# Kernel tuning notes

Hardware: AMD Instinct MI355X
Metric: run time of the kernel (lower is better)

## Reference

```python
import jax, jax.numpy as jnp
import numpy as np

HEADS = 8
DIM_HEAD = 40
SCALE = DIM_HEAD ** -0.5


def setup_inputs() -> dict:
    key = jax.random.key(0)
    ks = jax.random.split(key, 6)
    B, S, D = 2, 4096, 320  # batch, seq (64x64 latent), query_dim
    inner = HEADS * DIM_HEAD  # 320
    s = 0.02
    return {
        "x": jax.random.normal(ks[0], (B, S, D), jnp.float32),
        "Wq": jax.random.normal(ks[1], (inner, D), jnp.float32) * s,
        "Wk": jax.random.normal(ks[2], (inner, D), jnp.float32) * s,
        "Wv": jax.random.normal(ks[3], (inner, D), jnp.float32) * s,
        "Wout": jax.random.normal(ks[4], (D, inner), jnp.float32) * s,
        "bout": jnp.zeros((D,), jnp.float32),
    }


def _split_heads(t):
    # [B, S, h*d] -> [B, h, S, d]
    B, S, _ = t.shape
    return t.reshape(B, S, HEADS, DIM_HEAD).transpose(0, 2, 1, 3)


def reference(x, Wq, Wk, Wv, Wout, bout):
    # self-attention path (context=None): k/v come from x
    q = _split_heads(x @ Wq.T)  # [B,h,S,d]
    k = _split_heads(x @ Wk.T)
    v = _split_heads(x @ Wv.T)
    # scores: materialized O(S^2) attention as in the torch einsum
    attn = jax.nn.softmax(jnp.einsum('bhid,bhjd->bhij', q, k) * SCALE, axis=-1)
    out = jnp.einsum('bhij,bhjd->bhid', attn, v)  # [B,h,S,d]
    B, _, S, _ = out.shape
    out = out.transpose(0, 2, 1, 3).reshape(B, S, HEADS * DIM_HEAD)
    return out @ Wout.T + bout  # to_out (dropout=0 -> identity)
```

## Files before the change

### kernel.cpp

```cpp
#include <hip/hip_runtime.h>

#define HEADS 8
#define DHEAD 40
#define SEQ   4096
#define BATCH 2
#define INNER 320
#define NBH   16
#define QSCALE ((float)(0.15811388300841897 * 1.4426950408889634))

typedef _Float16 f16;
typedef __attribute__((ext_vector_type(2)))  __fp16   fp16x2;
typedef __attribute__((ext_vector_type(4)))  _Float16 half4;
typedef __attribute__((ext_vector_type(8)))  _Float16 half8;
typedef __attribute__((ext_vector_type(16))) float    f32x16;

#if __has_builtin(__builtin_amdgcn_exp2f)
#define EXP2F(x) __builtin_amdgcn_exp2f(x)
#else
#define EXP2F(x) exp2f(x)
#endif

union H8 { half8 h8; fp16x2 p2[4]; uint4 u4; };

#define XN4   (BATCH * SEQ * INNER / 4)
#define WQKV4 (3 * INNER * INNER / 4)
#define WOUT4 (INNER * INNER / 4)
#define CONV_TOTAL (XN4 + WQKV4 + WOUT4)

__global__ __launch_bounds__(256)
void convert_kernel(const float* __restrict__ x,
                    const float* __restrict__ Wq,
                    const float* __restrict__ Wk,
                    const float* __restrict__ Wv,
                    const float* __restrict__ Wout,
                    f16* __restrict__ xh, f16* __restrict__ wh,
                    f16* __restrict__ wouth)
{
    int i = blockIdx.x * 256 + threadIdx.x;
    if (i >= CONV_TOTAL) return;
    float4 v;
    f16* dst;
    float sc = 1.0f;
    if (i < XN4) {
        v = ((const float4*)x)[i];
        dst = xh + 4 * (size_t)i;
    } else if (i < XN4 + WQKV4) {
        int j = i - XN4;
        if (j < 25600)      { v = ((const float4*)Wq)[j]; sc = QSCALE; }
        else if (j < 51200) { v = ((const float4*)Wk)[j - 25600]; }
        else                { v = ((const float4*)Wv)[j - 51200]; }
        dst = wh + 4 * (size_t)j;
    } else {
        int j = i - XN4 - WQKV4;
        v = ((const float4*)Wout)[j];
        dst = wouth + 4 * (size_t)j;
    }
    H8 u;
    u.p2[0] = __builtin_amdgcn_cvt_pkrtz(v.x * sc, v.y * sc);
    u.p2[1] = __builtin_amdgcn_cvt_pkrtz(v.z * sc, v.w * sc);
    *(uint2*)dst = make_uint2(u.u4.x, u.u4.y);
}

#define QSTR 72

__global__ __launch_bounds__(256)
void qkv_gemm_kernel(const f16* __restrict__ xh, const f16* __restrict__ wh,
                     f16* __restrict__ q, f16* __restrict__ k,
                     f16* __restrict__ vt)
{
    __shared__ f16 lds[(64 + 192) * QSTR];
    f16* As = lds;
    f16* Bs = lds + 64 * QSTR;

    const int tid = threadIdx.x;
    const int nb0 = blockIdx.x * 64;
    const int m0  = blockIdx.y * 64;
    const int wave = tid >> 6, lane = tid & 63, m = lane & 31, half = lane >> 5;
    const int mw = wave >> 1, nw = wave & 1;

    f32x16 acc[3];
    #pragma unroll
    for (int i = 0; i < 16; i++) { acc[0][i] = 0.f; acc[1][i] = 0.f; acc[2][i] = 0.f; }

    for (int k0 = 0; k0 < 320; k0 += 64) {
        __syncthreads();
        #pragma unroll
        for (int u = 0; u < 2; u++) {
            int idx = tid + 256 * u;
            int r = idx >> 3, c8 = idx & 7;
            *(uint4*)&As[r * QSTR + c8 * 8] =
                *(const uint4*)&xh[(size_t)(m0 + r) * 320 + k0 + c8 * 8];
        }
        #pragma unroll
        for (int u = 0; u < 6; u++) {
            int idx = tid + 256 * u;
            int r = idx >> 3, c8 = idx & 7;
            int wr = (r >> 6) * 320 + nb0 + (r & 63);
            *(uint4*)&Bs[r * QSTR + c8 * 8] =
                *(const uint4*)&wh[(size_t)wr * 320 + k0 + c8 * 8];
        }
        __syncthreads();
        #pragma unroll
        for (int c = 0; c < 4; c++) {
            half8 a = *(const half8*)&As[(mw * 32 + m) * QSTR + c * 16 + half * 8];
            #pragma unroll
            for (int t = 0; t < 3; t++) {
                half8 bf = *(const half8*)&Bs[(nw * 96 + t * 32 + m) * QSTR + c * 16 + half * 8];
                acc[t] = __builtin_amdgcn_mfma_f32_32x32x16_f16(a, bf, acc[t], 0, 0, 0);
            }
        }
    }

    const int b = m0 >> 12, s0 = m0 & 4095;

    #pragma unroll
    for (int t = 0; t < 3; t++) {
        int st = nw * 3 + t;
        if (st < 4) {
            f16* dst = (st < 2) ? q : k;
            int col = nb0 + (st & 1) * 32 + m;
            int h  = (col * 205) >> 13;
            int dd = col - h * 40;
            #pragma unroll
            for (int reg = 0; reg < 16; reg++) {
                int crow = 4 * half + (reg & 3) + 8 * (reg >> 2);
                int mg = m0 + mw * 32 + crow;
                int bb = mg >> 12, s = mg & 4095;
                dst[((size_t)(bb * 8 + h) * SEQ + s) * DHEAD + dd] = (f16)acc[t][reg];
            }
        }
    }

    __syncthreads();
    f16* Ct = lds;
    if (nw == 1) {
        #pragma unroll
        for (int t = 1; t < 3; t++) {
            int vr0 = (t - 1) * 32 + m;
            #pragma unroll
            for (int g = 0; g < 4; g++) {
                half4 hh;
                hh.x = (f16)acc[t][4 * g + 0]; hh.y = (f16)acc[t][4 * g + 1];
                hh.z = (f16)acc[t][4 * g + 2]; hh.w = (f16)acc[t][4 * g + 3];
                *(half4*)&Ct[vr0 * QSTR + mw * 32 + 8 * g + 4 * half] = hh;
            }
        }
    }
    __syncthreads();
    #pragma unroll
    for (int u = 0; u < 4; u++) {
        int idx = tid + 256 * u;
        int rl = idx >> 4, c4 = idx & 15;
        int col = nb0 + rl;
        int h  = (col * 205) >> 13;
        int dd = col - h * 40;
        int w4 = c4 & 3;
        int c4p = (c4 & ~3) | ((w4 == 1) ? 2 : (w4 == 2) ? 1 : w4);
        *(uint2*)&vt[((size_t)(b * 8 + h) * DHEAD + dd) * SEQ + s0 + c4p * 4] =
            *(const uint2*)&Ct[rl * QSTR + c4 * 4];
    }
}

__global__ __launch_bounds__(256, 2)
void attn_kernel(const f16* __restrict__ q, const f16* __restrict__ k,
                 const f16* __restrict__ vt, f16* __restrict__ y)
{
    __shared__ __align__(16) unsigned char ldsbuf[33792];
    f16*   ldsh = (f16*)ldsbuf;
    float* ldsf = (float*)ldsbuf;

    const int tid = threadIdx.x;
    const int blk = blockIdx.x;
    const int xcd = blk & 7, slot = blk >> 3;
    const int bh = xcd * 2 + (slot >> 5), qt = slot & 31;
    const int b = bh >> 3, h = bh & 7;
    const int q0 = qt * 128;
    const int wave = tid >> 6, lane = tid & 63, m = lane & 31, half = lane >> 5;
    const int qp = wave >> 1, kh = wave & 1;
    const int x7 = m & 7;

    if (tid < 128) {
        int bsel = tid >> 6, r = tid & 63;
        *(uint4*)&ldsh[bsel * 8192 + r * 64 + 8 * (5 ^ (r & 7))] = make_uint4(0, 0, 0, 0);
    }
    #pragma unroll
    for (int u = 0; u < 2; u++) {
        int idx = tid + 256 * u;
        if (idx < 384) {
            int bsel = (idx >= 192) ? 1 : 0;
            int j = idx - bsel * 192;
            int r = 40 + (j >> 3), c = j & 7;
            uint4 val = (r == 40) ? make_uint4(0x3C003C00u, 0x3C003C00u, 0x3C003C00u, 0x3C003C00u)
                                  : make_uint4(0, 0, 0, 0);
            *(uint4*)&ldsh[bsel * 8192 + 4096 + r * 64 + 8 * (c ^ (r & 7))] = val;
        }
    }

    half8 zero8;
    #pragma unroll
    for (int j = 0; j < 8; j++) zero8[j] = (f16)0.0f;

    half8 qa[2][3];
    {
        const f16* qb = q + ((size_t)bh * SEQ + q0 + qp * 64 + m) * DHEAD;
        #pragma unroll
        for (int a = 0; a < 2; a++) {
            const f16* qr = qb + a * 32 * DHEAD;
            qa[a][0] = *(const half8*)&qr[half * 8];
            qa[a][1] = *(const half8*)&qr[16 + half * 8];
            qa[a][2] = (half == 1) ? zero8 : *(const half8*)&qr[32];
        }
    }

    f32x16 O[4];
    #pragma unroll
    for (int i = 0; i < 16; i++) { O[0][i] = 0.f; O[1][i] = 0.f; O[2][i] = 0.f; O[3][i] = 0.f; }
    f32x16 Zc;
    #pragma unroll
    for (int i = 0; i < 16; i++) Zc[i] = 0.f;

    const f16* kb = k  + (size_t)bh * SEQ * DHEAD;
    const f16* vb = vt + (size_t)bh * DHEAD * SEQ;

    const int krow0 = (tid * 205) >> 10,         kc0 = tid - krow0 * 5;
    const int krow1 = ((256 + tid) * 205) >> 10, kc1 = (256 + tid) - krow1 * 5;
    const int vrow0 = tid >> 3,        vc0 = tid & 7;
    const int vrow1 = (256 + tid) >> 3;
    const bool lo = (tid < 64);
    const int kdst0 = krow0 * 64 + 8 * (kc0 ^ (krow0 & 7));
    const int kdst1 = krow1 * 64 + 8 * (kc1 ^ (krow1 & 7));
    const int vdst0 = 4096 + vrow0 * 64 + 8 * (vc0 ^ (vrow0 & 7));
    const int vdst1 = 4096 + vrow1 * 64 + 8 * (vc0 ^ (vrow1 & 7));

    uint4 sk0, sk1, sv0, sv1;
    sk0 = *(const uint4*)&kb[krow0 * DHEAD + kc0 * 8];
    sv0 = *(const uint4*)&vb[(size_t)vrow0 * SEQ + vc0 * 8];
    if (lo) {
        sk1 = *(const uint4*)&kb[krow1 * DHEAD + kc1 * 8];
        sv1 = *(const uint4*)&vb[(size_t)vrow1 * SEQ + vc0 * 8];
    }

    for (int j0 = 0; j0 < SEQ; j0 += 64) {
        const int stg = ((j0 >> 6) & 1) * 8192;
        *(uint4*)&ldsh[stg + kdst0] = sk0;
        *(uint4*)&ldsh[stg + vdst0] = sv0;
        if (lo) {
            *(uint4*)&ldsh[stg + kdst1] = sk1;
            *(uint4*)&ldsh[stg + vdst1] = sv1;
        }
        __syncthreads();

        if (j0 + 64 < SEQ) {
            const int jn = j0 + 64;
            sk0 = *(const uint4*)&kb[(jn + krow0) * DHEAD + kc0 * 8];
            sv0 = *(const uint4*)&vb[(size_t)vrow0 * SEQ + jn + vc0 * 8];
            if (lo) {
                sk1 = *(const uint4*)&kb[(jn + krow1) * DHEAD + kc1 * 8];
                sv1 = *(const uint4*)&vb[(size_t)vrow1 * SEQ + jn + vc0 * 8];
            }
        }

        const f16* Kb = &ldsh[stg];
        const f16* Vb = &ldsh[stg + 4096];

        half8 kf[3];
        #pragma unroll
        for (int c = 0; c < 3; c++)
            kf[c] = *(const half8*)&Kb[(kh * 32 + m) * 64 + 8 * ((2 * c + half) ^ x7)];

        f32x16 Sa, Sb;
        __builtin_amdgcn_s_setprio(1);
        Sa = __builtin_amdgcn_mfma_f32_32x32x16_f16(kf[0], qa[0][0], Zc, 0, 0, 0);
        Sb = __builtin_amdgcn_mfma_f32_32x32x16_f16(kf[0], qa[1][0], Zc, 0, 0, 0);
        Sa = __builtin_amdgcn_mfma_f32_32x32x16_f16(kf[1], qa[0][1], Sa, 0, 0, 0);
        Sb = __builtin_amdgcn_mfma_f32_32x32x16_f16(kf[1], qa[1][1], Sb, 0, 0, 0);
        Sa = __builtin_amdgcn_mfma_f32_32x32x16_f16(kf[2], qa[0][2], Sa, 0, 0, 0);
        Sb = __builtin_amdgcn_mfma_f32_32x32x16_f16(kf[2], qa[1][2], Sb, 0, 0, 0);
        __builtin_amdgcn_s_setprio(0);

        half8 vf[2][2];
        #pragma unroll
        for (int c = 0; c < 2; c++) {
            vf[c][0] = *(const half8*)&Vb[m * 64        + 8 * ((4 * kh + 2 * c + half) ^ x7)];
            vf[c][1] = *(const half8*)&Vb[(32 + m) * 64 + 8 * ((4 * kh + 2 * c + half) ^ x7)];
        }

        H8 pa0, pa1, pb0, pb1;
        #pragma unroll
        for (int g = 0; g < 4; g++) {
            pa0.p2[g] = __builtin_amdgcn_cvt_pkrtz(EXP2F(Sa[2 * g]),     EXP2F(Sa[2 * g + 1]));
            pa1.p2[g] = __builtin_amdgcn_cvt_pkrtz(EXP2F(Sa[8 + 2 * g]), EXP2F(Sa[9 + 2 * g]));
            pb0.p2[g] = __builtin_amdgcn_cvt_pkrtz(EXP2F(Sb[2 * g]),     EXP2F(Sb[2 * g + 1]));
            pb1.p2[g] = __builtin_amdgcn_cvt_pkrtz(EXP2F(Sb[8 + 2 * g]), EXP2F(Sb[9 + 2 * g]));
        }

        __builtin_amdgcn_s_setprio(1);
        O[0] = __builtin_amdgcn_mfma_f32_32x32x16_f16(pa0.h8, vf[0][0], O[0], 0, 0, 0);
        O[1] = __builtin_amdgcn_mfma_f32_32x32x16_f16(pa0.h8, vf[0][1], O[1], 0, 0, 0);
        O[2] = __builtin_amdgcn_mfma_f32_32x32x16_f16(pb0.h8, vf[0][0], O[2], 0, 0, 0);
        O[3] = __builtin_amdgcn_mfma_f32_32x32x16_f16(pb0.h8, vf[0][1], O[3], 0, 0, 0);
        O[0] = __builtin_amdgcn_mfma_f32_32x32x16_f16(pa1.h8, vf[1][0], O[0], 0, 0, 0);
        O[1] = __builtin_amdgcn_mfma_f32_32x32x16_f16(pa1.h8, vf[1][1], O[1], 0, 0, 0);
        O[2] = __builtin_amdgcn_mfma_f32_32x32x16_f16(pb1.h8, vf[1][0], O[2], 0, 0, 0);
        O[3] = __builtin_amdgcn_mfma_f32_32x32x16_f16(pb1.h8, vf[1][1], O[3], 0, 0, 0);
        __builtin_amdgcn_s_setprio(0);
    }

    __syncthreads();
    if (kh == 1) {
        #pragma unroll
        for (int a = 0; a < 2; a++)
            #pragma unroll
            for (int t = 0; t < 2; t++)
                #pragma unroll
                for (int reg = 0; reg < 16; reg++) {
                    int row = 4 * half + (reg & 3) + 8 * (reg >> 2);
                    ldsf[(qp * 64 + a * 32 + row) * 66 + t * 32 + m] = O[a * 2 + t][reg];
                }
    }
    __syncthreads();
    if (kh == 0) {
        #pragma unroll
        for (int a = 0; a < 2; a++) {
            #pragma unroll
            for (int t = 0; t < 2; t++)
                #pragma unroll
                for (int reg = 0; reg < 16; reg++) {
                    int row = 4 * half + (reg & 3) + 8 * (reg >> 2);
                    O[a * 2 + t][reg] += ldsf[(qp * 64 + a * 32 + row) * 66 + t * 32 + m];
                }
            #pragma unroll
            for (int reg = 0; reg < 16; reg++) {
                float l = __shfl(O[a * 2 + 1][reg], 8 + 32 * half, 64);
                float rinv = 1.0f / l;
                int row = 4 * half + (reg & 3) + 8 * (reg >> 2);
                f16* yr = y + ((size_t)b * SEQ + q0 + qp * 64 + a * 32 + row) * INNER + h * DHEAD;
                yr[m] = (f16)(O[a * 2 + 0][reg] * rinv);
                if (m < 8) yr[32 + m] = (f16)(O[a * 2 + 1][reg] * rinv);
            }
        }
    }
}

#define ASTR 72

__global__ __launch_bounds__(256)
void out_proj_kernel(const f16* __restrict__ y, const f16* __restrict__ wouth,
                     const float* __restrict__ bout, float* __restrict__ out)
{
    __shared__ f16 lds[(128 + 64) * ASTR];
    f16* As = lds;
    f16* Bs = lds + 128 * ASTR;

    const int tid = threadIdx.x;
    const int m0 = blockIdx.y * 128;
    const int n0 = blockIdx.x * 64;
    const int wave = tid >> 6, lane = tid & 63, m = lane & 31, half = lane >> 5;

    f32x16 acc[2];
    #pragma unroll
    for (int i = 0; i < 16; i++) { acc[0][i] = 0.f; acc[1][i] = 0.f; }

    for (int k0 = 0; k0 < 320; k0 += 64) {
        __syncthreads();
        #pragma unroll
        for (int u = 0; u < 4; u++) {
            int idx = tid + 256 * u;
            int r = idx >> 3, c8 = idx & 7;
            *(uint4*)&As[r * ASTR + c8 * 8] =
                *(const uint4*)&y[(size_t)(m0 + r) * 320 + k0 + c8 * 8];
        }
        #pragma unroll
        for (int u = 0; u < 2; u++) {
            int idx = tid + 256 * u;
            int r = idx >> 3, c8 = idx & 7;
            *(uint4*)&Bs[r * ASTR + c8 * 8] =
                *(const uint4*)&wouth[(size_t)(n0 + r) * 320 + k0 + c8 * 8];
        }
        __syncthreads();
        #pragma unroll
        for (int c = 0; c < 4; c++) {
            half8 a  = *(const half8*)&As[(wave * 32 + m) * ASTR + c * 16 + half * 8];
            half8 b0 = *(const half8*)&Bs[m * ASTR + c * 16 + half * 8];
            half8 b1 = *(const half8*)&Bs[(32 + m) * ASTR + c * 16 + half * 8];
            acc[0] = __builtin_amdgcn_mfma_f32_32x32x16_f16(a, b0, acc[0], 0, 0, 0);
            acc[1] = __builtin_amdgcn_mfma_f32_32x32x16_f16(a, b1, acc[1], 0, 0, 0);
        }
    }

    #pragma unroll
    for (int nt = 0; nt < 2; nt++) {
        int n = n0 + nt * 32 + m;
        float bias = bout[n];
        #pragma unroll
        for (int reg = 0; reg < 16; reg++) {
            int crow = 4 * half + (reg & 3) + 8 * (reg >> 2);
            out[(size_t)(m0 + wave * 32 + crow) * 320 + n] = acc[nt][reg] + bias;
        }
    }
}

extern "C" void kernel_launch(void* const* d_in, const int* in_sizes, int n_in,
                              void* d_out, int out_size, void* d_ws, size_t ws_size,
                              hipStream_t stream)
{
    const float* x    = (const float*)d_in[0];
    const float* Wq   = (const float*)d_in[1];
    const float* Wk   = (const float*)d_in[2];
    const float* Wv   = (const float*)d_in[3];
    const float* Wout = (const float*)d_in[4];
    const float* bout = (const float*)d_in[5];
    float* out = (float*)d_out;

    unsigned char* ws = (unsigned char*)d_ws;
    f16* xh    = (f16*)(ws);
    f16* wh    = (f16*)(ws +  5242880);
    f16* wouth = (f16*)(ws +  5857280);
    f16* qd    = (f16*)(ws +  6062080);
    f16* kd    = (f16*)(ws + 11304960);
    f16* vtd   = (f16*)(ws + 16547840);
    f16* yd    = (f16*)(ws + 21790720);

    convert_kernel <<<2960,         256, 0, stream>>>(x, Wq, Wk, Wv, Wout, xh, wh, wouth);
    qkv_gemm_kernel<<<dim3(5, 128), 256, 0, stream>>>(xh, wh, qd, kd, vtd);
    attn_kernel    <<<512,          256, 0, stream>>>(qd, kd, vtd, yd);
    out_proj_kernel<<<dim3(5, 64),  256, 0, stream>>>(yd, wouth, bout, out);
}
```

Before: 162.3 us.

## Double K/V tile to 128 keys in attention and register-prefetch GEMM tiles

The attention kernel now stages 128 keys per iteration instead of 64 in a larger double-buffered LDS region, and processes two 64-key sub-blocks per barrier. This halves the barrier and loop overhead count. The QKV and output-projection GEMMs now prefetch the next k-slice into registers while the current slice is computed, overlapping global loads with MFMA work. The larger LDS footprint (64KB) may cut attention occupancy below the two blocks per CU requested by the launch bounds, and the extra live registers add pressure.

```diff
diff --git a/kernel.cpp b/kernel.cpp
--- a/kernel.cpp
+++ b/kernel.cpp
@@ -19,6 +19,8 @@
 #else
 #define EXP2F(x) exp2f(x)
 #endif
+
+#define MFMA16(a, b, c) __builtin_amdgcn_mfma_f32_32x32x16_f16(a, b, c, 0, 0, 0)
 
 union H8 { half8 h8; fp16x2 p2[4]; uint4 u4; };
 
@@ -78,35 +80,52 @@
     const int wave = tid >> 6, lane = tid & 63, m = lane & 31, half = lane >> 5;
     const int mw = wave >> 1, nw = wave & 1;
 
+    const int ar = tid >> 3, ac8 = tid & 7;
+    const int ar1 = (256 + tid) >> 3;
+    int br[6], bwr[6];
+    #pragma unroll
+    for (int u = 0; u < 6; u++) {
+        int idx = tid + 256 * u;
+        int r = idx >> 3;
+        br[u] = r;
+        bwr[u] = (r >> 6) * 320 + nb0 + (r & 63);
+    }
+
     f32x16 acc[3];
     #pragma unroll
     for (int i = 0; i < 16; i++) { acc[0][i] = 0.f; acc[1][i] = 0.f; acc[2][i] = 0.f; }
+
+    uint4 pa0, pa1, pb[6];
+    pa0 = *(const uint4*)&xh[(size_t)(m0 + ar)  * 320 + ac8 * 8];
+    pa1 = *(const uint4*)&xh[(size_t)(m0 + ar1) * 320 + ac8 * 8];
+    #pragma unroll
+    for (int u = 0; u < 6; u++)
+        pb[u] = *(const uint4*)&wh[(size_t)bwr[u] * 320 + ac8 * 8];
 
     for (int k0 = 0; k0 < 320; k0 += 64) {
         __syncthreads();
-        #pragma unroll
-        for (int u = 0; u < 2; u++) {
-            int idx = tid + 256 * u;
-            int r = idx >> 3, c8 = idx & 7;
-            *(uint4*)&As[r * QSTR + c8 * 8] =
-                *(const uint4*)&xh[(size_t)(m0 + r) * 320 + k0 + c8 * 8];
-        }
-        #pragma unroll
-        for (int u = 0; u < 6; u++) {
-            int idx = tid + 256 * u;
-            int r = idx >> 3, c8 = idx & 7;
-            int wr = (r >> 6) * 320 + nb0 + (r & 63);
-            *(uint4*)&Bs[r * QSTR + c8 * 8] =
-                *(const uint4*)&wh[(size_t)wr * 320 + k0 + c8 * 8];
-        }
+        *(uint4*)&As[ar  * QSTR + ac8 * 8] = pa0;
+        *(uint4*)&As[ar1 * QSTR + ac8 * 8] = pa1;
+        #pragma unroll
+        for (int u = 0; u < 6; u++)
+            *(uint4*)&Bs[br[u] * QSTR + ac8 * 8] = pb[u];
         __syncthreads();
+
+        if (k0 + 64 < 320) {
+            pa0 = *(const uint4*)&xh[(size_t)(m0 + ar)  * 320 + k0 + 64 + ac8 * 8];
+            pa1 = *(const uint4*)&xh[(size_t)(m0 + ar1) * 320 + k0 + 64 + ac8 * 8];
+            #pragma unroll
+            for (int u = 0; u < 6; u++)
+                pb[u] = *(const uint4*)&wh[(size_t)bwr[u] * 320 + k0 + 64 + ac8 * 8];
+        }
+
         #pragma unroll
         for (int c = 0; c < 4; c++) {
             half8 a = *(const half8*)&As[(mw * 32 + m) * QSTR + c * 16 + half * 8];
             #pragma unroll
             for (int t = 0; t < 3; t++) {
                 half8 bf = *(const half8*)&Bs[(nw * 96 + t * 32 + m) * QSTR + c * 16 + half * 8];
-                acc[t] = __builtin_amdgcn_mfma_f32_32x32x16_f16(a, bf, acc[t], 0, 0, 0);
+                acc[t] = MFMA16(a, bf, acc[t]);
             }
         }
     }
@@ -165,7 +184,7 @@
 void attn_kernel(const f16* __restrict__ q, const f16* __restrict__ k,
                  const f16* __restrict__ vt, f16* __restrict__ y)
 {
-    __shared__ __align__(16) unsigned char ldsbuf[33792];
+    __shared__ __align__(16) unsigned char ldsbuf[65536];
     f16*   ldsh = (f16*)ldsbuf;
     float* ldsf = (float*)ldsbuf;
 
@@ -179,21 +198,19 @@
     const int qp = wave >> 1, kh = wave & 1;
     const int x7 = m & 7;
 
-    if (tid < 128) {
-        int bsel = tid >> 6, r = tid & 63;
-        *(uint4*)&ldsh[bsel * 8192 + r * 64 + 8 * (5 ^ (r & 7))] = make_uint4(0, 0, 0, 0);
-    }
-    #pragma unroll
-    for (int u = 0; u < 2; u++) {
+    {
+        int bsel = tid >> 7, r = tid & 127;
+        *(uint4*)&ldsh[bsel * 16384 + r * 64 + 8 * (5 ^ (r & 7))] = make_uint4(0, 0, 0, 0);
+    }
+    #pragma unroll
+    for (int u = 0; u < 3; u++) {
         int idx = tid + 256 * u;
-        if (idx < 384) {
-            int bsel = (idx >= 192) ? 1 : 0;
-            int j = idx - bsel * 192;
-            int r = 40 + (j >> 3), c = j & 7;
-            uint4 val = (r == 40) ? make_uint4(0x3C003C00u, 0x3C003C00u, 0x3C003C00u, 0x3C003C00u)
-                                  : make_uint4(0, 0, 0, 0);
-            *(uint4*)&ldsh[bsel * 8192 + 4096 + r * 64 + 8 * (c ^ (r & 7))] = val;
-        }
+        int bsel = (idx >= 384) ? 1 : 0;
+        int j = idx - bsel * 384;
+        int r = 40 + (j >> 4), c = j & 15;
+        uint4 val = (r == 40) ? make_uint4(0x3C003C00u, 0x3C003C00u, 0x3C003C00u, 0x3C003C00u)
+                              : make_uint4(0, 0, 0, 0);
+        *(uint4*)&ldsh[bsel * 16384 + 8192 + r * 128 + 8 * (c ^ (r & 7))] = val;
     }
 
     half8 zero8;
@@ -222,87 +239,123 @@
     const f16* kb = k  + (size_t)bh * SEQ * DHEAD;
     const f16* vb = vt + (size_t)bh * DHEAD * SEQ;
 
-    const int krow0 = (tid * 205) >> 10,         kc0 = tid - krow0 * 5;
-    const int krow1 = ((256 + tid) * 205) >> 10, kc1 = (256 + tid) - krow1 * 5;
-    const int vrow0 = tid >> 3,        vc0 = tid & 7;
-    const int vrow1 = (256 + tid) >> 3;
-    const bool lo = (tid < 64);
-    const int kdst0 = krow0 * 64 + 8 * (kc0 ^ (krow0 & 7));
-    const int kdst1 = krow1 * 64 + 8 * (kc1 ^ (krow1 & 7));
-    const int vdst0 = 4096 + vrow0 * 64 + 8 * (vc0 ^ (vrow0 & 7));
-    const int vdst1 = 4096 + vrow1 * 64 + 8 * (vc0 ^ (vrow1 & 7));
-
-    uint4 sk0, sk1, sv0, sv1;
-    sk0 = *(const uint4*)&kb[krow0 * DHEAD + kc0 * 8];
-    sv0 = *(const uint4*)&vb[(size_t)vrow0 * SEQ + vc0 * 8];
-    if (lo) {
-        sk1 = *(const uint4*)&kb[krow1 * DHEAD + kc1 * 8];
-        sv1 = *(const uint4*)&vb[(size_t)vrow1 * SEQ + vc0 * 8];
-    }
-
-    for (int j0 = 0; j0 < SEQ; j0 += 64) {
-        const int stg = ((j0 >> 6) & 1) * 8192;
-        *(uint4*)&ldsh[stg + kdst0] = sk0;
-        *(uint4*)&ldsh[stg + vdst0] = sv0;
-        if (lo) {
-            *(uint4*)&ldsh[stg + kdst1] = sk1;
-            *(uint4*)&ldsh[stg + vdst1] = sv1;
+    int krow[3], kc[3], kdst[3], vrow[3], vc[3], vdst[3];
+    #pragma unroll
+    for (int u = 0; u < 3; u++) {
+        int idx = tid + 256 * u;
+        int r = (idx * 205) >> 10, c = idx - r * 5;
+        krow[u] = r; kc[u] = c;
+        kdst[u] = r * 64 + 8 * (c ^ (r & 7));
+        int vr = idx >> 4, vcc = idx & 15;
+        vrow[u] = vr; vc[u] = vcc;
+        vdst[u] = 8192 + vr * 128 + 8 * (vcc ^ (vr & 7));
+    }
+    const bool full3 = (tid < 128);
+
+    uint4 sk[3], sv[3];
+    #pragma unroll
+    for (int u = 0; u < 2; u++) {
+        sk[u] = *(const uint4*)&kb[(size_t)krow[u] * DHEAD + kc[u] * 8];
+        sv[u] = *(const uint4*)&vb[(size_t)vrow[u] * SEQ + vc[u] * 8];
+    }
+    if (full3) {
+        sk[2] = *(const uint4*)&kb[(size_t)krow[2] * DHEAD + kc[2] * 8];
+        sv[2] = *(const uint4*)&vb[(size_t)vrow[2] * SEQ + vc[2] * 8];
+    }
+
+    for (int j0 = 0; j0 < SEQ; j0 += 128) {
+        const int stg = ((j0 >> 7) & 1) * 16384;
+        #pragma unroll
+        for (int u = 0; u < 2; u++) {
+            *(uint4*)&ldsh[stg + kdst[u]] = sk[u];
+            *(uint4*)&ldsh[stg + vdst[u]] = sv[u];
+        }
+        if (full3) {
+            *(uint4*)&ldsh[stg + kdst[2]] = sk[2];
+            *(uint4*)&ldsh[stg + vdst[2]] = sv[2];
         }
         __syncthreads();
 
-        if (j0 + 64 < SEQ) {
-            const int jn = j0 + 64;
-            sk0 = *(const uint4*)&kb[(jn + krow0) * DHEAD + kc0 * 8];
-            sv0 = *(const uint4*)&vb[(size_t)vrow0 * SEQ + jn + vc0 * 8];
-            if (lo) {
-                sk1 = *(const uint4*)&kb[(jn + krow1) * DHEAD + kc1 * 8];
-                sv1 = *(const uint4*)&vb[(size_t)vrow1 * SEQ + jn + vc0 * 8];
+        if (j0 + 128 < SEQ) {
+            const int jn = j0 + 128;
+            #pragma unroll
+            for (int u = 0; u < 2; u++) {
+                sk[u] = *(const uint4*)&kb[(size_t)(jn + krow[u]) * DHEAD + kc[u] * 8];
+                sv[u] = *(const uint4*)&vb[(size_t)vrow[u] * SEQ + jn + vc[u] * 8];
+            }
+            if (full3) {
+                sk[2] = *(const uint4*)&kb[(size_t)(jn + krow[2]) * DHEAD + kc[2] * 8];
+                sv[2] = *(const uint4*)&vb[(size_t)vrow[2] * SEQ + jn + vc[2] * 8];
             }
         }
 
         const f16* Kb = &ldsh[stg];
-        const f16* Vb = &ldsh[stg + 4096];
-
-        half8 kf[3];
-        #pragma unroll
-        for (int c = 0; c < 3; c++)
-            kf[c] = *(const half8*)&Kb[(kh * 32 + m) * 64 + 8 * ((2 * c + half) ^ x7)];
-
-        f32x16 Sa, Sb;
+        const f16* Vb = &ldsh[stg + 8192];
+
+        half8 kfA[3], kfB[3];
+        #pragma unroll
+        for (int c = 0; c < 3; c++) {
+            kfA[c] = *(const half8*)&Kb[(kh * 32 + m) * 64      + 8 * ((2 * c + half) ^ x7)];
+            kfB[c] = *(const half8*)&Kb[(64 + kh * 32 + m) * 64 + 8 * ((2 * c + half) ^ x7)];
+        }
+
+        f32x16 SaA, SbA, SaB, SbB;
         __builtin_amdgcn_s_setprio(1);
-        Sa = __builtin_amdgcn_mfma_f32_32x32x16_f16(kf[0], qa[0][0], Zc, 0, 0, 0);
-        Sb = __builtin_amdgcn_mfma_f32_32x32x16_f16(kf[0], qa[1][0], Zc, 0, 0, 0);
-        Sa = __builtin_amdgcn_mfma_f32_32x32x16_f16(kf[1], qa[0][1], Sa, 0, 0, 0);
-        Sb = __builtin_amdgcn_mfma_f32_32x32x16_f16(kf[1], qa[1][1], Sb, 0, 0, 0);
-        Sa = __builtin_amdgcn_mfma_f32_32x32x16_f16(kf[2], qa[0][2], Sa, 0, 0, 0);
-        Sb = __builtin_amdgcn_mfma_f32_32x32x16_f16(kf[2], qa[1][2], Sb, 0, 0, 0);
+        SaA = MFMA16(kfA[0], qa[0][0], Zc);  SbA = MFMA16(kfA[0], qa[1][0], Zc);
+        SaA = MFMA16(kfA[1], qa[0][1], SaA); SbA = MFMA16(kfA[1], qa[1][1], SbA);
+        SaA = MFMA16(kfA[2], qa[0][2], SaA); SbA = MFMA16(kfA[2], qa[1][2], SbA);
+        SaB = MFMA16(kfB[0], qa[0][0], Zc);  SbB = MFMA16(kfB[0], qa[1][0], Zc);
+        SaB = MFMA16(kfB[1], qa[0][1], SaB); SbB = MFMA16(kfB[1], qa[1][1], SbB);
+        SaB = MFMA16(kfB[2], qa[0][2], SaB); SbB = MFMA16(kfB[2], qa[1][2], SbB);
         __builtin_amdgcn_s_setprio(0);
 
-        half8 vf[2][2];
+        half8 vfA[2][2];
         #pragma unroll
         for (int c = 0; c < 2; c++) {
-            vf[c][0] = *(const half8*)&Vb[m * 64        + 8 * ((4 * kh + 2 * c + half) ^ x7)];
-            vf[c][1] = *(const half8*)&Vb[(32 + m) * 64 + 8 * ((4 * kh + 2 * c + half) ^ x7)];
-        }
-
+            vfA[c][0] = *(const half8*)&Vb[m * 128        + 8 * ((4 * kh + 2 * c + half) ^ x7)];
+            vfA[c][1] = *(const half8*)&Vb[(32 + m) * 128 + 8 * ((4 * kh + 2 * c + half) ^ x7)];
+        }
         H8 pa0, pa1, pb0, pb1;
         #pragma unroll
         for (int g = 0; g < 4; g++) {
-            pa0.p2[g] = __builtin_amdgcn_cvt_pkrtz(EXP2F(Sa[2 * g]),     EXP2F(Sa[2 * g + 1]));
-            pa1.p2[g] = __builtin_amdgcn_cvt_pkrtz(EXP2F(Sa[8 + 2 * g]), EXP2F(Sa[9 + 2 * g]));
-            pb0.p2[g] = __builtin_amdgcn_cvt_pkrtz(EXP2F(Sb[2 * g]),     EXP2F(Sb[2 * g + 1]));
-            pb1.p2[g] = __builtin_amdgcn_cvt_pkrtz(EXP2F(Sb[8 + 2 * g]), EXP2F(Sb[9 + 2 * g]));
-        }
-
+            pa0.p2[g] = __builtin_amdgcn_cvt_pkrtz(EXP2F(SaA[2 * g]),     EXP2F(SaA[2 * g + 1]));
+            pa1.p2[g] = __builtin_amdgcn_cvt_pkrtz(EXP2F(SaA[8 + 2 * g]), EXP2F(SaA[9 + 2 * g]));
+            pb0.p2[g] = __builtin_amdgcn_cvt_pkrtz(EXP2F(SbA[2 * g]),     EXP2F(SbA[2 * g + 1]));
+            pb1.p2[g] = __builtin_amdgcn_cvt_pkrtz(EXP2F(SbA[8 + 2 * g]), EXP2F(SbA[9 + 2 * g]));
+        }
         __builtin_amdgcn_s_setprio(1);
-        O[0] = __builtin_amdgcn_mfma_f32_32x32x16_f16(pa0.h8, vf[0][0], O[0], 0, 0, 0);
-        O[1] = __builtin_amdgcn_mfma_f32_32x32x16_f16(pa0.h8, vf[0][1], O[1], 0, 0, 0);
-        O[2] = __builtin_amdgcn_mfma_f32_32x32x16_f16(pb0.h8, vf[0][0], O[2], 0, 0, 0);
-        O[3] = __builtin_amdgcn_mfma_f32_32x32x16_f16(pb0.h8, vf[0][1], O[3], 0, 0, 0);
-        O[0] = __builtin_amdgcn_mfma_f32_32x32x16_f16(pa1.h8, vf[1][0], O[0], 0, 0, 0);
-        O[1] = __builtin_amdgcn_mfma_f32_32x32x16_f16(pa1.h8, vf[1][1], O[1], 0, 0, 0);
-        O[2] = __builtin_amdgcn_mfma_f32_32x32x16_f16(pb1.h8, vf[1][0], O[2], 0, 0, 0);
-        O[3] = __builtin_amdgcn_mfma_f32_32x32x16_f16(pb1.h8, vf[1][1], O[3], 0, 0, 0);
+        O[0] = MFMA16(pa0.h8, vfA[0][0], O[0]);
+        O[1] = MFMA16(pa0.h8, vfA[0][1], O[1]);
+        O[2] = MFMA16(pb0.h8, vfA[0][0], O[2]);
+        O[3] = MFMA16(pb0.h8, vfA[0][1], O[3]);
+        O[0] = MFMA16(pa1.h8, vfA[1][0], O[0]);
+        O[1] = MFMA16(pa1.h8, vfA[1][1], O[1]);
+        O[2] = MFMA16(pb1.h8, vfA[1][0], O[2]);
+        O[3] = MFMA16(pb1.h8, vfA[1][1], O[3]);
+        __builtin_amdgcn_s_setprio(0);
+
+        half8 vfB[2][2];
+        #pragma unroll
+        for (int c = 0; c < 2; c++) {
+            vfB[c][0] = *(const half8*)&Vb[m * 128        + 8 * ((8 + 4 * kh + 2 * c + half) ^ x7)];
+            vfB[c][1] = *(const half8*)&Vb[(32 + m) * 128 + 8 * ((8 + 4 * kh + 2 * c + half) ^ x7)];
+        }
+        #pragma unroll
+        for (int g = 0; g < 4; g++) {
+            pa0.p2[g] = __builtin_amdgcn_cvt_pkrtz(EXP2F(SaB[2 * g]),     EXP2F(SaB[2 * g + 1]));
+            pa1.p2[g] = __builtin_amdgcn_cvt_pkrtz(EXP2F(SaB[8 + 2 * g]), EXP2F(SaB[9 + 2 * g]));
+            pb0.p2[g] = __builtin_amdgcn_cvt_pkrtz(EXP2F(SbB[2 * g]),     EXP2F(SbB[2 * g + 1]));
+            pb1.p2[g] = __builtin_amdgcn_cvt_pkrtz(EXP2F(SbB[8 + 2 * g]), EXP2F(SbB[9 + 2 * g]));
+        }
+        __builtin_amdgcn_s_setprio(1);
+        O[0] = MFMA16(pa0.h8, vfB[0][0], O[0]);
+        O[1] = MFMA16(pa0.h8, vfB[0][1], O[1]);
+        O[2] = MFMA16(pb0.h8, vfB[0][0], O[2]);
+        O[3] = MFMA16(pb0.h8, vfB[0][1], O[3]);
+        O[0] = MFMA16(pa1.h8, vfB[1][0], O[0]);
+        O[1] = MFMA16(pa1.h8, vfB[1][1], O[1]);
+        O[2] = MFMA16(pb1.h8, vfB[1][0], O[2]);
+        O[3] = MFMA16(pb1.h8, vfB[1][1], O[3]);
         __builtin_amdgcn_s_setprio(0);
     }
 
@@ -357,34 +410,46 @@
     const int n0 = blockIdx.x * 64;
     const int wave = tid >> 6, lane = tid & 63, m = lane & 31, half = lane >> 5;
 
+    const int r0 = tid >> 3, c8 = tid & 7;
+
     f32x16 acc[2];
     #pragma unroll
     for (int i = 0; i < 16; i++) { acc[0][i] = 0.f; acc[1][i] = 0.f; }
+
+    uint4 pa[4], pb[2];
+    #pragma unroll
+    for (int u = 0; u < 4; u++)
+        pa[u] = *(const uint4*)&y[(size_t)(m0 + r0 + 32 * u) * 320 + c8 * 8];
+    #pragma unroll
+    for (int u = 0; u < 2; u++)
+        pb[u] = *(const uint4*)&wouth[(size_t)(n0 + r0 + 32 * u) * 320 + c8 * 8];
 
     for (int k0 = 0; k0 < 320; k0 += 64) {
         __syncthreads();
         #pragma unroll
-        for (int u = 0; u < 4; u++) {
-            int idx = tid + 256 * u;
-            int r = idx >> 3, c8 = idx & 7;
-            *(uint4*)&As[r * ASTR + c8 * 8] =
-                *(const uint4*)&y[(size_t)(m0 + r) * 320 + k0 + c8 * 8];
-        }
-        #pragma unroll
-        for (int u = 0; u < 2; u++) {
-            int idx = tid + 256 * u;
-            int r = idx >> 3, c8 = idx & 7;
-            *(uint4*)&Bs[r * ASTR + c8 * 8] =
-                *(const uint4*)&wouth[(size_t)(n0 + r) * 320 + k0 + c8 * 8];
-        }
+        for (int u = 0; u < 4; u++)
+            *(uint4*)&As[(r0 + 32 * u) * ASTR + c8 * 8] = pa[u];
+        #pragma unroll
+        for (int u = 0; u < 2; u++)
+            *(uint4*)&Bs[(r0 + 32 * u) * ASTR + c8 * 8] = pb[u];
         __syncthreads();
+
+        if (k0 + 64 < 320) {
+            #pragma unroll
+            for (int u = 0; u < 4; u++)
+                pa[u] = *(const uint4*)&y[(size_t)(m0 + r0 + 32 * u) * 320 + k0 + 64 + c8 * 8];
+            #pragma unroll
+            for (int u = 0; u < 2; u++)
+                pb[u] = *(const uint4*)&wouth[(size_t)(n0 + r0 + 32 * u) * 320 + k0 + 64 + c8 * 8];
+        }
+
         #pragma unroll
         for (int c = 0; c < 4; c++) {
             half8 a  = *(const half8*)&As[(wave * 32 + m) * ASTR + c * 16 + half * 8];
             half8 b0 = *(const half8*)&Bs[m * ASTR + c * 16 + half * 8];
             half8 b1 = *(const half8*)&Bs[(32 + m) * ASTR + c * 16 + half * 8];
-            acc[0] = __builtin_amdgcn_mfma_f32_32x32x16_f16(a, b0, acc[0], 0, 0, 0);
-            acc[1] = __builtin_amdgcn_mfma_f32_32x32x16_f16(a, b1, acc[1], 0, 0, 0);
+            acc[0] = MFMA16(a, b0, acc[0]);
+            acc[1] = MFMA16(a, b1, acc[1]);
         }
     }
 
```

Result: slower. 236.6 us (+45.7%).
